# Performance work log

Hardware: AMD Instinct MI355X
Metric: run time of the kernel (lower is better)

## Reference

```python
import jax, jax.numpy as jnp
import numpy as np

B, H, T, D = 2, 16, 2048, 64


def setup_inputs() -> dict:
    key = jax.random.key(0)
    kq, kk, kv, km = jax.random.split(key, 4)
    q = jax.random.normal(kq, (B, H, T, D), dtype=jnp.float32)
    k = jax.random.normal(kk, (B, H, T, D), dtype=jnp.float32)
    v = jax.random.normal(kv, (B, H, T, D), dtype=jnp.float32)
    # boolean mask, True = masked out (broadcast over batch and heads)
    mask = jax.random.randint(km, (1, 1, T, T), 0, 2).astype(jnp.bool_)
    return {"q": q, "k": k, "v": v, "mask": mask}


def reference(q, k, v, mask):
    scale = q.shape[-1] ** (-0.5)
    # [B,H,T,T] score matrix (materialized, as in the original)
    scores = jnp.einsum("bhqd,bhkd->bhqk", q, k) * scale
    scores = jnp.where(mask, jnp.float32(-10000.0), scores)
    attn = jax.nn.softmax(scores, axis=-1)
    attn = jnp.where(mask, jnp.float32(0.0), attn)
    return jnp.einsum("bhqk,bhkd->bhqd", attn, v)
```

## Files before the change

### kernel.cpp

```cpp
#include <hip/hip_runtime.h>
#include <hip/hip_bf16.h>

typedef __bf16 bf16x8 __attribute__((ext_vector_type(8)));
typedef __bf16 bf16x4 __attribute__((ext_vector_type(4)));
typedef float  f32x4  __attribute__((ext_vector_type(4)));
typedef short  s16x4  __attribute__((ext_vector_type(4)));

#define T_SEQ 2048
#define D_HEAD 64
#define BH_N 32
#define SCALE_LOG2 0.18033688011112042f

#define WS_KBF ((size_t)0)
#define WS_VTB ((size_t)8u<<20)
#define WS_MB  ((size_t)16u<<20)

static __device__ inline f32x4 mfma16(bf16x4 a, bf16x4 b, f32x4 c) {
#if __has_builtin(__builtin_amdgcn_mfma_f32_16x16x16_bf16)
    return __builtin_amdgcn_mfma_f32_16x16x16_bf16(a, b, c, 0, 0, 0);
#else
    s16x4 ai = __builtin_bit_cast(s16x4, a);
    s16x4 bi = __builtin_bit_cast(s16x4, b);
    return __builtin_amdgcn_mfma_f32_16x16x16bf16_1k(ai, bi, c, 0, 0, 0);
#endif
}


__global__ __launch_bounds__(256) void prep_kv(const float* __restrict__ k,
                                               const float* __restrict__ v,
                                               __bf16* __restrict__ kb,
                                               __bf16* __restrict__ vt) {
    __shared__ __bf16 t[64][72];
    const int bh = blockIdx.y, tt = blockIdx.x, tid = threadIdx.x;

    {
        const size_t base = ((size_t)bh * T_SEQ + tt * 64 + (tid >> 2)) * D_HEAD + (tid & 3) * 16;
        const float4 a0 = *(const float4*)(k + base);
        const float4 a1 = *(const float4*)(k + base + 4);
        const float4 a2 = *(const float4*)(k + base + 8);
        const float4 a3 = *(const float4*)(k + base + 12);
        bf16x8 w0, w1;
        w0[0]=(__bf16)a0.x; w0[1]=(__bf16)a0.y; w0[2]=(__bf16)a0.z; w0[3]=(__bf16)a0.w;
        w0[4]=(__bf16)a1.x; w0[5]=(__bf16)a1.y; w0[6]=(__bf16)a1.z; w0[7]=(__bf16)a1.w;
        w1[0]=(__bf16)a2.x; w1[1]=(__bf16)a2.y; w1[2]=(__bf16)a2.z; w1[3]=(__bf16)a2.w;
        w1[4]=(__bf16)a3.x; w1[5]=(__bf16)a3.y; w1[6]=(__bf16)a3.z; w1[7]=(__bf16)a3.w;
        *(bf16x8*)(kb + base)     = w0;
        *(bf16x8*)(kb + base + 8) = w1;
    }
    {
        const int tr = tid >> 4, c4 = (tid & 15) * 4;
        const float* src = v + ((size_t)bh * T_SEQ + tt * 64) * D_HEAD;
#pragma unroll
        for (int p = 0; p < 4; ++p) {
            const int row = p * 16 + tr;
            const float4 f = *(const float4*)(src + row * D_HEAD + c4);
            t[c4+0][row] = (__bf16)f.x; t[c4+1][row] = (__bf16)f.y;
            t[c4+2][row] = (__bf16)f.z; t[c4+3][row] = (__bf16)f.w;
        }
        __syncthreads();
        const int d = tid >> 2, seg = tid & 3;
        const bf16x8 a = *(bf16x8*)&t[d][seg * 16];
        const bf16x8 b = *(bf16x8*)&t[d][seg * 16 + 8];
        __bf16* dst = vt + ((size_t)bh * D_HEAD + d) * T_SEQ + tt * 64 + seg * 16;
        *(bf16x8*)dst = a; *(bf16x8*)(dst + 8) = b;
    }
}

__global__ void mpack(const int* __restrict__ m, unsigned long long* __restrict__ mb) {
    const int i = blockIdx.x * 256 + threadIdx.x;
    const unsigned long long b = __ballot(m[i] != 0);
    if ((threadIdx.x & 63) == 0) mb[i >> 6] = b;
}


__global__ __launch_bounds__(128, 2) void attn5(
    const float* __restrict__ q, const __bf16* __restrict__ kb,
    const __bf16* __restrict__ vt, const unsigned long long* __restrict__ mb,
    float* __restrict__ out)
{
    const int qt = blockIdx.x;
    const int bh = blockIdx.y;
    const int tid = threadIdx.x, wave = tid >> 6, lane = tid & 63;
    const int g = lane >> 4, ln = lane & 15;

    __shared__ __align__(16) __bf16 Kl[2][64 * 64];
    __shared__ __align__(16) __bf16 Vl[2][64 * 64];
    __shared__ float ls[2][32];

    const int qw = qt * 64 + wave * 32;

    bf16x8 qf[2][2];
#pragma unroll
    for (int qs = 0; qs < 2; ++qs) {
        const float* qp = q + ((size_t)bh * T_SEQ + qw + qs * 16 + ln) * D_HEAD + g * 8;
#pragma unroll
        for (int kc = 0; kc < 2; ++kc) {
            const float4 f0 = *(const float4*)(qp + kc * 32);
            const float4 f1 = *(const float4*)(qp + kc * 32 + 4);
            qf[qs][kc][0]=(__bf16)(f0.x*SCALE_LOG2); qf[qs][kc][1]=(__bf16)(f0.y*SCALE_LOG2);
            qf[qs][kc][2]=(__bf16)(f0.z*SCALE_LOG2); qf[qs][kc][3]=(__bf16)(f0.w*SCALE_LOG2);
            qf[qs][kc][4]=(__bf16)(f1.x*SCALE_LOG2); qf[qs][kc][5]=(__bf16)(f1.y*SCALE_LOG2);
            qf[qs][kc][6]=(__bf16)(f1.z*SCALE_LOG2); qf[qs][kc][7]=(__bf16)(f1.w*SCALE_LOG2);
        }
    }

    f32x4 o[2][4];
#pragma unroll
    for (int qs = 0; qs < 2; ++qs)
#pragma unroll
        for (int mt = 0; mt < 4; ++mt) o[qs][mt] = (f32x4){0.f, 0.f, 0.f, 0.f};
    float lsum[2] = {0.f, 0.f};

    const int kr = tid >> 1, h = tid & 1;
    const int kwb = kr * 128, ke = kr & 7, ve = kr & 15;
    const __bf16* kbase = kb + (size_t)bh * T_SEQ * D_HEAD;
    const __bf16* vbase = vt + (size_t)bh * D_HEAD * T_SEQ;
    const unsigned long long* mrow0 = mb + (size_t)(qw + ln) * 32;
    const unsigned long long* mrow1 = mb + (size_t)(qw + 16 + ln) * 32;

    char* KlB = (char*)Kl;
    char* VlB = (char*)Vl;

    bf16x8 kn[4], vn[4];

    {
        const __bf16* kp = kbase + (size_t)kr * D_HEAD + h * 32;
        kn[0]=*(const bf16x8*)kp;      kn[1]=*(const bf16x8*)(kp+8);
        kn[2]=*(const bf16x8*)(kp+16); kn[3]=*(const bf16x8*)(kp+24);
        const __bf16* vp = vbase + (size_t)kr * T_SEQ + h * 32;
        vn[0]=*(const bf16x8*)vp;      vn[1]=*(const bf16x8*)(vp+8);
        vn[2]=*(const bf16x8*)(vp+16); vn[3]=*(const bf16x8*)(vp+24);
    }
    unsigned long long mw0 = mrow0[0], mw1 = mrow1[0];
    {
        char* KB = KlB; char* VB = VlB;
#pragma unroll
        for (int i = 0; i < 4; ++i)
            *(bf16x8*)(KB + kwb + (((4*h + i) ^ ke) << 4)) = kn[i];
#pragma unroll
        for (int i = 0; i < 4; ++i) {
            const bf16x4 lo = __builtin_shufflevector(vn[i], vn[i], 0, 1, 2, 3);
            const bf16x4 hi = __builtin_shufflevector(vn[i], vn[i], 4, 5, 6, 7);
            *(bf16x4*)(VB + kwb + (((8*h + 2*i)     ^ ve) << 3)) = lo;
            *(bf16x4*)(VB + kwb + (((8*h + 2*i + 1) ^ ve) << 3)) = hi;
        }
    }
    __syncthreads();

    const int rbK = ln * 128 + ((g ^ (ln & 7)) << 4);

    for (int kt = 0; kt < T_SEQ / 64; ++kt) {
        const int b = kt & 1;
        unsigned long long mn0 = 0, mn1 = 0;
        if (kt < 31) {
            const __bf16* kp = kbase + (size_t)((kt + 1) * 64 + kr) * D_HEAD + h * 32;
            kn[0]=*(const bf16x8*)kp;      kn[1]=*(const bf16x8*)(kp+8);
            kn[2]=*(const bf16x8*)(kp+16); kn[3]=*(const bf16x8*)(kp+24);
            const __bf16* vp = vbase + (size_t)kr * T_SEQ + (kt + 1) * 64 + h * 32;
            vn[0]=*(const bf16x8*)vp;      vn[1]=*(const bf16x8*)(vp+8);
            vn[2]=*(const bf16x8*)(vp+16); vn[3]=*(const bf16x8*)(vp+24);
            mn0 = mrow0[kt + 1]; mn1 = mrow1[kt + 1];
        }

        const char* KB = KlB + b * 8192;
        const char* VB = VlB + b * 8192;

        const unsigned long long s0 = mw0 >> (g * 4), s1 = mw1 >> (g * 4);
        const unsigned int mlo[2] = {(unsigned)s0, (unsigned)s1};
        const unsigned int mhi[2] = {(unsigned)(s0 >> 32), (unsigned)(s1 >> 32)};

        bf16x4 pa[2][4];
#pragma unroll
        for (int nt = 0; nt < 4; ++nt) {
            const bf16x8 a0 = *(const bf16x8*)(KB + nt * 2048 + rbK);
            const bf16x8 a1 = *(const bf16x8*)(KB + nt * 2048 + (rbK ^ 64));
#pragma unroll
            for (int qs = 0; qs < 2; ++qs) {
                f32x4 c = (f32x4){0.f, 0.f, 0.f, 0.f};
                c = __builtin_amdgcn_mfma_f32_16x16x32_bf16(a0, qf[qs][0], c, 0, 0, 0);
                c = __builtin_amdgcn_mfma_f32_16x16x32_bf16(a1, qf[qs][1], c, 0, 0, 0);
                const unsigned int bits = (nt < 2) ? mlo[qs] : mhi[qs];
                float p[4];
#pragma unroll
                for (int r = 0; r < 4; ++r) {
                    const float e = exp2f(c[r]);
                    p[r] = (bits & (1u << ((nt & 1) * 16 + r))) ? 0.f : e;
                }
                lsum[qs] += (p[0] + p[1]) + (p[2] + p[3]);
                pa[qs][nt] = (bf16x4){ (__bf16)p[0], (__bf16)p[1], (__bf16)p[2], (__bf16)p[3] };
            }
        }

#pragma unroll
        for (int mt = 0; mt < 4; ++mt) {
            bf16x4 vf[4];
#pragma unroll
            for (int nt = 0; nt < 4; ++nt)
                vf[nt] = *(const bf16x4*)(VB + (mt * 16 + ln) * 128 + (((nt * 4 + g) ^ (ln & 15)) << 3));
#pragma unroll
            for (int qs = 0; qs < 2; ++qs)
#pragma unroll
                for (int nt = 0; nt < 4; ++nt)
                    o[qs][mt] = mfma16(pa[qs][nt], vf[nt], o[qs][mt]);
        }

        if (kt < 31) {
            char* KB1 = KlB + (b ^ 1) * 8192;
            char* VB1 = VlB + (b ^ 1) * 8192;
#pragma unroll
            for (int i = 0; i < 4; ++i)
                *(bf16x8*)(KB1 + kwb + (((4*h + i) ^ ke) << 4)) = kn[i];
#pragma unroll
            for (int i = 0; i < 4; ++i) {
                const bf16x4 lo = __builtin_shufflevector(vn[i], vn[i], 0, 1, 2, 3);
                const bf16x4 hi = __builtin_shufflevector(vn[i], vn[i], 4, 5, 6, 7);
                *(bf16x4*)(VB1 + kwb + (((8*h + 2*i)     ^ ve) << 3)) = lo;
                *(bf16x4*)(VB1 + kwb + (((8*h + 2*i + 1) ^ ve) << 3)) = hi;
            }
        }
        __syncthreads();
        mw0 = mn0; mw1 = mn1;
    }

#pragma unroll
    for (int qs = 0; qs < 2; ++qs) {
        float l = lsum[qs];
        l += __shfl_xor(l, 16, 64);
        l += __shfl_xor(l, 32, 64);
        const float inv = (l > 0.f) ? (1.f / l) : 0.f;
        if (g == 0) ls[wave][qs * 16 + ln] = inv;
    }
#pragma unroll
    for (int qs = 0; qs < 2; ++qs) {
#pragma unroll
        for (int r = 0; r < 4; ++r) {
            const float iv = ls[wave][qs * 16 + g * 4 + r];
            float* op = out + ((size_t)bh * T_SEQ + qw + qs * 16 + g * 4 + r) * D_HEAD + ln;
#pragma unroll
            for (int mt = 0; mt < 4; ++mt)
                op[mt * 16] = o[qs][mt][r] * iv;
        }
    }
}

extern "C" void kernel_launch(void* const* d_in, const int* in_sizes, int n_in,
                              void* d_out, int out_size, void* d_ws, size_t ws_size,
                              hipStream_t stream) {
    const float* q    = (const float*)d_in[0];
    const float* k    = (const float*)d_in[1];
    const float* v    = (const float*)d_in[2];
    const int*   mask = (const int*)d_in[3];
    float*       out  = (float*)d_out;

    __bf16* kbf = (__bf16*)((char*)d_ws + WS_KBF);
    __bf16* vtb = (__bf16*)((char*)d_ws + WS_VTB);
    unsigned long long* mbw = (unsigned long long*)((char*)d_ws + WS_MB);

    prep_kv<<<dim3(T_SEQ / 64, BH_N), 256, 0, stream>>>(k, v, kbf, vtb);
    mpack<<<(T_SEQ * T_SEQ) / 256, 256, 0, stream>>>(mask, mbw);
    attn5<<<dim3(T_SEQ / 64, BH_N), 128, 0, stream>>>(q, kbf, vtb, mbw, out);
}
```

Before: 185.7 us.

## Split attention block into four waves of 16 queries and sum rows via MFMA

The attention kernel now runs 256 threads (four waves) per 64-query block, each wave owning 16 query rows instead of 32. That halves per-wave accumulator registers and aims for more waves in flight. The row-sum of probabilities is computed with an extra MFMA against a ones vector, replacing the scalar sum, cross-lane shuffles and shared-memory broadcast. In exchange, each K fragment read from LDS now feeds only one query subtile, so LDS traffic per MFMA goes up, and the row-sum MFMAs add matrix work.

```diff
diff --git a/kernel.cpp b/kernel.cpp
--- a/kernel.cpp
+++ b/kernel.cpp
@@ -73,7 +73,7 @@
 }
 
 
-__global__ __launch_bounds__(128, 2) void attn5(
+__global__ __launch_bounds__(256, 4) void attn6(
     const float* __restrict__ q, const __bf16* __restrict__ kb,
     const __bf16* __restrict__ vt, const unsigned long long* __restrict__ mb,
     float* __restrict__ out)
@@ -85,64 +85,57 @@
 
     __shared__ __align__(16) __bf16 Kl[2][64 * 64];
     __shared__ __align__(16) __bf16 Vl[2][64 * 64];
-    __shared__ float ls[2][32];
-
-    const int qw = qt * 64 + wave * 32;
-
-    bf16x8 qf[2][2];
-#pragma unroll
-    for (int qs = 0; qs < 2; ++qs) {
-        const float* qp = q + ((size_t)bh * T_SEQ + qw + qs * 16 + ln) * D_HEAD + g * 8;
+
+    const int qw = qt * 64 + wave * 16;
+
+    bf16x8 qf[2];
+    {
+        const float* qp = q + ((size_t)bh * T_SEQ + qw + ln) * D_HEAD + g * 8;
 #pragma unroll
         for (int kc = 0; kc < 2; ++kc) {
             const float4 f0 = *(const float4*)(qp + kc * 32);
             const float4 f1 = *(const float4*)(qp + kc * 32 + 4);
-            qf[qs][kc][0]=(__bf16)(f0.x*SCALE_LOG2); qf[qs][kc][1]=(__bf16)(f0.y*SCALE_LOG2);
-            qf[qs][kc][2]=(__bf16)(f0.z*SCALE_LOG2); qf[qs][kc][3]=(__bf16)(f0.w*SCALE_LOG2);
-            qf[qs][kc][4]=(__bf16)(f1.x*SCALE_LOG2); qf[qs][kc][5]=(__bf16)(f1.y*SCALE_LOG2);
-            qf[qs][kc][6]=(__bf16)(f1.z*SCALE_LOG2); qf[qs][kc][7]=(__bf16)(f1.w*SCALE_LOG2);
-        }
-    }
-
-    f32x4 o[2][4];
-#pragma unroll
-    for (int qs = 0; qs < 2; ++qs)
-#pragma unroll
-        for (int mt = 0; mt < 4; ++mt) o[qs][mt] = (f32x4){0.f, 0.f, 0.f, 0.f};
-    float lsum[2] = {0.f, 0.f};
-
-    const int kr = tid >> 1, h = tid & 1;
+            qf[kc][0]=(__bf16)(f0.x*SCALE_LOG2); qf[kc][1]=(__bf16)(f0.y*SCALE_LOG2);
+            qf[kc][2]=(__bf16)(f0.z*SCALE_LOG2); qf[kc][3]=(__bf16)(f0.w*SCALE_LOG2);
+            qf[kc][4]=(__bf16)(f1.x*SCALE_LOG2); qf[kc][5]=(__bf16)(f1.y*SCALE_LOG2);
+            qf[kc][6]=(__bf16)(f1.z*SCALE_LOG2); qf[kc][7]=(__bf16)(f1.w*SCALE_LOG2);
+        }
+    }
+
+    f32x4 o[4];
+#pragma unroll
+    for (int mt = 0; mt < 4; ++mt) o[mt] = (f32x4){0.f, 0.f, 0.f, 0.f};
+    f32x4 osum = (f32x4){0.f, 0.f, 0.f, 0.f};
+    const bf16x4 ones = { (__bf16)1.0f, (__bf16)1.0f, (__bf16)1.0f, (__bf16)1.0f };
+
+    const int kr = tid >> 2, qd = tid & 3;
     const int kwb = kr * 128, ke = kr & 7, ve = kr & 15;
     const __bf16* kbase = kb + (size_t)bh * T_SEQ * D_HEAD;
     const __bf16* vbase = vt + (size_t)bh * D_HEAD * T_SEQ;
-    const unsigned long long* mrow0 = mb + (size_t)(qw + ln) * 32;
-    const unsigned long long* mrow1 = mb + (size_t)(qw + 16 + ln) * 32;
+    const unsigned long long* mrow = mb + (size_t)(qw + ln) * 32;
 
     char* KlB = (char*)Kl;
     char* VlB = (char*)Vl;
 
-    bf16x8 kn[4], vn[4];
-
-    {
-        const __bf16* kp = kbase + (size_t)kr * D_HEAD + h * 32;
-        kn[0]=*(const bf16x8*)kp;      kn[1]=*(const bf16x8*)(kp+8);
-        kn[2]=*(const bf16x8*)(kp+16); kn[3]=*(const bf16x8*)(kp+24);
-        const __bf16* vp = vbase + (size_t)kr * T_SEQ + h * 32;
-        vn[0]=*(const bf16x8*)vp;      vn[1]=*(const bf16x8*)(vp+8);
-        vn[2]=*(const bf16x8*)(vp+16); vn[3]=*(const bf16x8*)(vp+24);
-    }
-    unsigned long long mw0 = mrow0[0], mw1 = mrow1[0];
-    {
-        char* KB = KlB; char* VB = VlB;
-#pragma unroll
-        for (int i = 0; i < 4; ++i)
-            *(bf16x8*)(KB + kwb + (((4*h + i) ^ ke) << 4)) = kn[i];
-#pragma unroll
-        for (int i = 0; i < 4; ++i) {
+    bf16x8 kn[2], vn[2];
+
+    {
+        const __bf16* kp = kbase + (size_t)kr * D_HEAD + qd * 16;
+        kn[0] = *(const bf16x8*)kp; kn[1] = *(const bf16x8*)(kp + 8);
+        const __bf16* vp = vbase + (size_t)kr * T_SEQ + qd * 16;
+        vn[0] = *(const bf16x8*)vp; vn[1] = *(const bf16x8*)(vp + 8);
+    }
+    unsigned long long mw = mrow[0];
+    {
+#pragma unroll
+        for (int i = 0; i < 2; ++i)
+            *(bf16x8*)(KlB + kwb + (((2*qd + i) ^ ke) << 4)) = kn[i];
+#pragma unroll
+        for (int i = 0; i < 2; ++i) {
             const bf16x4 lo = __builtin_shufflevector(vn[i], vn[i], 0, 1, 2, 3);
             const bf16x4 hi = __builtin_shufflevector(vn[i], vn[i], 4, 5, 6, 7);
-            *(bf16x4*)(VB + kwb + (((8*h + 2*i)     ^ ve) << 3)) = lo;
-            *(bf16x4*)(VB + kwb + (((8*h + 2*i + 1) ^ ve) << 3)) = hi;
+            *(bf16x4*)(VlB + kwb + (((4*qd + 2*i)     ^ ve) << 3)) = lo;
+            *(bf16x4*)(VlB + kwb + (((4*qd + 2*i + 1) ^ ve) << 3)) = hi;
         }
     }
     __syncthreads();
@@ -151,45 +144,42 @@
 
     for (int kt = 0; kt < T_SEQ / 64; ++kt) {
         const int b = kt & 1;
-        unsigned long long mn0 = 0, mn1 = 0;
+        unsigned long long mn = 0;
         if (kt < 31) {
-            const __bf16* kp = kbase + (size_t)((kt + 1) * 64 + kr) * D_HEAD + h * 32;
-            kn[0]=*(const bf16x8*)kp;      kn[1]=*(const bf16x8*)(kp+8);
-            kn[2]=*(const bf16x8*)(kp+16); kn[3]=*(const bf16x8*)(kp+24);
-            const __bf16* vp = vbase + (size_t)kr * T_SEQ + (kt + 1) * 64 + h * 32;
-            vn[0]=*(const bf16x8*)vp;      vn[1]=*(const bf16x8*)(vp+8);
-            vn[2]=*(const bf16x8*)(vp+16); vn[3]=*(const bf16x8*)(vp+24);
-            mn0 = mrow0[kt + 1]; mn1 = mrow1[kt + 1];
+            const __bf16* kp = kbase + (size_t)((kt + 1) * 64 + kr) * D_HEAD + qd * 16;
+            kn[0] = *(const bf16x8*)kp; kn[1] = *(const bf16x8*)(kp + 8);
+            const __bf16* vp = vbase + (size_t)kr * T_SEQ + (kt + 1) * 64 + qd * 16;
+            vn[0] = *(const bf16x8*)vp; vn[1] = *(const bf16x8*)(vp + 8);
+            mn = mrow[kt + 1];
         }
 
         const char* KB = KlB + b * 8192;
         const char* VB = VlB + b * 8192;
 
-        const unsigned long long s0 = mw0 >> (g * 4), s1 = mw1 >> (g * 4);
-        const unsigned int mlo[2] = {(unsigned)s0, (unsigned)s1};
-        const unsigned int mhi[2] = {(unsigned)(s0 >> 32), (unsigned)(s1 >> 32)};
-
-        bf16x4 pa[2][4];
+        const unsigned long long s = mw >> (g * 4);
+        const unsigned int mlo = (unsigned)s, mhi = (unsigned)(s >> 32);
+
+        bf16x4 pa[4];
 #pragma unroll
         for (int nt = 0; nt < 4; ++nt) {
             const bf16x8 a0 = *(const bf16x8*)(KB + nt * 2048 + rbK);
             const bf16x8 a1 = *(const bf16x8*)(KB + nt * 2048 + (rbK ^ 64));
-#pragma unroll
-            for (int qs = 0; qs < 2; ++qs) {
-                f32x4 c = (f32x4){0.f, 0.f, 0.f, 0.f};
-                c = __builtin_amdgcn_mfma_f32_16x16x32_bf16(a0, qf[qs][0], c, 0, 0, 0);
-                c = __builtin_amdgcn_mfma_f32_16x16x32_bf16(a1, qf[qs][1], c, 0, 0, 0);
-                const unsigned int bits = (nt < 2) ? mlo[qs] : mhi[qs];
-                float p[4];
-#pragma unroll
-                for (int r = 0; r < 4; ++r) {
-                    const float e = exp2f(c[r]);
-                    p[r] = (bits & (1u << ((nt & 1) * 16 + r))) ? 0.f : e;
-                }
-                lsum[qs] += (p[0] + p[1]) + (p[2] + p[3]);
-                pa[qs][nt] = (bf16x4){ (__bf16)p[0], (__bf16)p[1], (__bf16)p[2], (__bf16)p[3] };
+            f32x4 c = (f32x4){0.f, 0.f, 0.f, 0.f};
+            c = __builtin_amdgcn_mfma_f32_16x16x32_bf16(a0, qf[0], c, 0, 0, 0);
+            c = __builtin_amdgcn_mfma_f32_16x16x32_bf16(a1, qf[1], c, 0, 0, 0);
+            const unsigned int bits = (nt < 2) ? mlo : mhi;
+            float p[4];
+#pragma unroll
+            for (int r = 0; r < 4; ++r) {
+                const float e = exp2f(c[r]);
+                p[r] = (bits & (1u << ((nt & 1) * 16 + r))) ? 0.f : e;
             }
-        }
+            pa[nt] = (bf16x4){ (__bf16)p[0], (__bf16)p[1], (__bf16)p[2], (__bf16)p[3] };
+        }
+
+#pragma unroll
+        for (int nt = 0; nt < 4; ++nt)
+            osum = mfma16(pa[nt], ones, osum);
 
 #pragma unroll
         for (int mt = 0; mt < 4; ++mt) {
@@ -198,48 +188,36 @@
             for (int nt = 0; nt < 4; ++nt)
                 vf[nt] = *(const bf16x4*)(VB + (mt * 16 + ln) * 128 + (((nt * 4 + g) ^ (ln & 15)) << 3));
 #pragma unroll
-            for (int qs = 0; qs < 2; ++qs)
-#pragma unroll
-                for (int nt = 0; nt < 4; ++nt)
-                    o[qs][mt] = mfma16(pa[qs][nt], vf[nt], o[qs][mt]);
+            for (int nt = 0; nt < 4; ++nt)
+                o[mt] = mfma16(pa[nt], vf[nt], o[mt]);
         }
 
         if (kt < 31) {
             char* KB1 = KlB + (b ^ 1) * 8192;
             char* VB1 = VlB + (b ^ 1) * 8192;
 #pragma unroll
-            for (int i = 0; i < 4; ++i)
-                *(bf16x8*)(KB1 + kwb + (((4*h + i) ^ ke) << 4)) = kn[i];
-#pragma unroll
-            for (int i = 0; i < 4; ++i) {
+            for (int i = 0; i < 2; ++i)
+                *(bf16x8*)(KB1 + kwb + (((2*qd + i) ^ ke) << 4)) = kn[i];
+#pragma unroll
+            for (int i = 0; i < 2; ++i) {
                 const bf16x4 lo = __builtin_shufflevector(vn[i], vn[i], 0, 1, 2, 3);
                 const bf16x4 hi = __builtin_shufflevector(vn[i], vn[i], 4, 5, 6, 7);
-                *(bf16x4*)(VB1 + kwb + (((8*h + 2*i)     ^ ve) << 3)) = lo;
-                *(bf16x4*)(VB1 + kwb + (((8*h + 2*i + 1) ^ ve) << 3)) = hi;
+                *(bf16x4*)(VB1 + kwb + (((4*qd + 2*i)     ^ ve) << 3)) = lo;
+                *(bf16x4*)(VB1 + kwb + (((4*qd + 2*i + 1) ^ ve) << 3)) = hi;
             }
         }
         __syncthreads();
-        mw0 = mn0; mw1 = mn1;
-    }
-
-#pragma unroll
-    for (int qs = 0; qs < 2; ++qs) {
-        float l = lsum[qs];
-        l += __shfl_xor(l, 16, 64);
-        l += __shfl_xor(l, 32, 64);
+        mw = mn;
+    }
+
+#pragma unroll
+    for (int r = 0; r < 4; ++r) {
+        const float l = osum[r];
         const float inv = (l > 0.f) ? (1.f / l) : 0.f;
-        if (g == 0) ls[wave][qs * 16 + ln] = inv;
-    }
-#pragma unroll
-    for (int qs = 0; qs < 2; ++qs) {
-#pragma unroll
-        for (int r = 0; r < 4; ++r) {
-            const float iv = ls[wave][qs * 16 + g * 4 + r];
-            float* op = out + ((size_t)bh * T_SEQ + qw + qs * 16 + g * 4 + r) * D_HEAD + ln;
-#pragma unroll
-            for (int mt = 0; mt < 4; ++mt)
-                op[mt * 16] = o[qs][mt][r] * iv;
-        }
+        float* op = out + ((size_t)bh * T_SEQ + qw + g * 4 + r) * D_HEAD + ln;
+#pragma unroll
+        for (int mt = 0; mt < 4; ++mt)
+            op[mt * 16] = o[mt][r] * inv;
     }
 }
 
@@ -258,5 +236,5 @@
 
     prep_kv<<<dim3(T_SEQ / 64, BH_N), 256, 0, stream>>>(k, v, kbf, vtb);
     mpack<<<(T_SEQ * T_SEQ) / 256, 256, 0, stream>>>(mask, mbw);
-    attn5<<<dim3(T_SEQ / 64, BH_N), 128, 0, stream>>>(q, kbf, vtb, mbw, out);
-}
+    attn6<<<dim3(T_SEQ / 64, BH_N), 256, 0, stream>>>(q, kbf, vtb, mbw, out);
+}
```

Result: faster. 177.5 us (-4.4%).

## Split key tile across wave pairs with 256-thread blocks and LDS reduction

Applied to the files above, without the earlier changes.

Doubles the block to four waves, with pairs of waves each handling half of every 64-key tile for the same 32 queries, then sums the partial outputs and row sums through shared memory at the end. Row sums are now computed with an MFMA against a ones vector instead of scalar adds. Masking uses a branch-free bitwise AND, and exp2 goes through the hardware intrinsic. The V shared-memory layout is reswizzled for single 16-byte reads. This aims to raise occupancy and cut per-wave VALU work. The cost is an extra epilogue reduction through LDS and more blocks competing for LDS.

```diff
diff --git a/kernel.cpp b/kernel.cpp
--- a/kernel.cpp
+++ b/kernel.cpp
@@ -25,6 +25,14 @@
 #endif
 }
 
+static __device__ inline float fast_exp2(float x) {
+#if __has_builtin(__builtin_amdgcn_exp2f)
+    return __builtin_amdgcn_exp2f(x);
+#else
+    return exp2f(x);
+#endif
+}
+
 
 __global__ __launch_bounds__(256) void prep_kv(const float* __restrict__ k,
                                                const float* __restrict__ v,
@@ -32,7 +40,6 @@
                                                __bf16* __restrict__ vt) {
     __shared__ __bf16 t[64][72];
     const int bh = blockIdx.y, tt = blockIdx.x, tid = threadIdx.x;
-
     {
         const size_t base = ((size_t)bh * T_SEQ + tt * 64 + (tid >> 2)) * D_HEAD + (tid & 3) * 16;
         const float4 a0 = *(const float4*)(k + base);
@@ -73,7 +80,7 @@
 }
 
 
-__global__ __launch_bounds__(128, 2) void attn5(
+__global__ __launch_bounds__(256, 4) void attn8(
     const float* __restrict__ q, const __bf16* __restrict__ kb,
     const __bf16* __restrict__ vt, const unsigned long long* __restrict__ mb,
     float* __restrict__ out)
@@ -82,21 +89,24 @@
     const int bh = blockIdx.y;
     const int tid = threadIdx.x, wave = tid >> 6, lane = tid & 63;
     const int g = lane >> 4, ln = lane & 15;
-
-    __shared__ __align__(16) __bf16 Kl[2][64 * 64];
-    __shared__ __align__(16) __bf16 Vl[2][64 * 64];
-    __shared__ float ls[2][32];
-
-    const int qw = qt * 64 + wave * 32;
+    const int qp = wave & 1, kh = wave >> 1;
+
+    __shared__ __align__(16) char smem[33280];
+    char* KlB = smem;
+    char* VlB = smem + 16384;
+    float* Ep = (float*)smem;
+    float* Os = (float*)(smem + 32768);
+
+    const int qw = qt * 64 + qp * 32;
 
     bf16x8 qf[2][2];
 #pragma unroll
     for (int qs = 0; qs < 2; ++qs) {
-        const float* qp = q + ((size_t)bh * T_SEQ + qw + qs * 16 + ln) * D_HEAD + g * 8;
+        const float* qpt = q + ((size_t)bh * T_SEQ + qw + qs * 16 + ln) * D_HEAD + g * 8;
 #pragma unroll
         for (int kc = 0; kc < 2; ++kc) {
-            const float4 f0 = *(const float4*)(qp + kc * 32);
-            const float4 f1 = *(const float4*)(qp + kc * 32 + 4);
+            const float4 f0 = *(const float4*)(qpt + kc * 32);
+            const float4 f1 = *(const float4*)(qpt + kc * 32 + 4);
             qf[qs][kc][0]=(__bf16)(f0.x*SCALE_LOG2); qf[qs][kc][1]=(__bf16)(f0.y*SCALE_LOG2);
             qf[qs][kc][2]=(__bf16)(f0.z*SCALE_LOG2); qf[qs][kc][3]=(__bf16)(f0.w*SCALE_LOG2);
             qf[qs][kc][4]=(__bf16)(f1.x*SCALE_LOG2); qf[qs][kc][5]=(__bf16)(f1.y*SCALE_LOG2);
@@ -109,114 +119,111 @@
     for (int qs = 0; qs < 2; ++qs)
 #pragma unroll
         for (int mt = 0; mt < 4; ++mt) o[qs][mt] = (f32x4){0.f, 0.f, 0.f, 0.f};
-    float lsum[2] = {0.f, 0.f};
-
-    const int kr = tid >> 1, h = tid & 1;
-    const int kwb = kr * 128, ke = kr & 7, ve = kr & 15;
+    f32x4 osum[2] = { (f32x4){0.f,0.f,0.f,0.f}, (f32x4){0.f,0.f,0.f,0.f} };
+    const bf16x4 ones = { (__bf16)1.0f, (__bf16)1.0f, (__bf16)1.0f, (__bf16)1.0f };
+
+    const int kr = tid >> 2, qd = tid & 3;
+    const int kwb = kr * 128, ke = kr & 7;
     const __bf16* kbase = kb + (size_t)bh * T_SEQ * D_HEAD;
     const __bf16* vbase = vt + (size_t)bh * D_HEAD * T_SEQ;
     const unsigned long long* mrow0 = mb + (size_t)(qw + ln) * 32;
     const unsigned long long* mrow1 = mb + (size_t)(qw + 16 + ln) * 32;
 
-    char* KlB = (char*)Kl;
-    char* VlB = (char*)Vl;
-
-    bf16x8 kn[4], vn[4];
-
-    {
-        const __bf16* kp = kbase + (size_t)kr * D_HEAD + h * 32;
-        kn[0]=*(const bf16x8*)kp;      kn[1]=*(const bf16x8*)(kp+8);
-        kn[2]=*(const bf16x8*)(kp+16); kn[3]=*(const bf16x8*)(kp+24);
-        const __bf16* vp = vbase + (size_t)kr * T_SEQ + h * 32;
-        vn[0]=*(const bf16x8*)vp;      vn[1]=*(const bf16x8*)(vp+8);
-        vn[2]=*(const bf16x8*)(vp+16); vn[3]=*(const bf16x8*)(vp+24);
+    bf16x8 kn[2], vn[2];
+
+    {
+        const __bf16* kp = kbase + (size_t)kr * D_HEAD + qd * 16;
+        kn[0] = *(const bf16x8*)kp; kn[1] = *(const bf16x8*)(kp + 8);
+        const __bf16* vp = vbase + (size_t)kr * T_SEQ + qd * 16;
+        vn[0] = *(const bf16x8*)vp; vn[1] = *(const bf16x8*)(vp + 8);
     }
     unsigned long long mw0 = mrow0[0], mw1 = mrow1[0];
     {
-        char* KB = KlB; char* VB = VlB;
-#pragma unroll
-        for (int i = 0; i < 4; ++i)
-            *(bf16x8*)(KB + kwb + (((4*h + i) ^ ke) << 4)) = kn[i];
-#pragma unroll
-        for (int i = 0; i < 4; ++i) {
-            const bf16x4 lo = __builtin_shufflevector(vn[i], vn[i], 0, 1, 2, 3);
-            const bf16x4 hi = __builtin_shufflevector(vn[i], vn[i], 4, 5, 6, 7);
-            *(bf16x4*)(VB + kwb + (((8*h + 2*i)     ^ ve) << 3)) = lo;
-            *(bf16x4*)(VB + kwb + (((8*h + 2*i + 1) ^ ve) << 3)) = hi;
-        }
+        *(bf16x8*)(KlB + kwb + (((2*qd + 0) ^ ke) << 4)) = kn[0];
+        *(bf16x8*)(KlB + kwb + (((2*qd + 1) ^ ke) << 4)) = kn[1];
+#pragma unroll
+        for (int c = 0; c < 2; ++c)
+#pragma unroll
+            for (int gg = 0; gg < 2; ++gg) {
+                const int g2 = c * 2 + gg;
+                const int gran = (g2 << 1) | (qd >> 1);
+                const bf16x4 part = gg ? __builtin_shufflevector(vn[c], vn[c], 4,5,6,7)
+                                       : __builtin_shufflevector(vn[c], vn[c], 0,1,2,3);
+                *(bf16x4*)(VlB + kwb + ((gran ^ ke) << 4) + ((qd & 1) << 3)) = part;
+            }
     }
     __syncthreads();
-
-    const int rbK = ln * 128 + ((g ^ (ln & 7)) << 4);
 
     for (int kt = 0; kt < T_SEQ / 64; ++kt) {
         const int b = kt & 1;
         unsigned long long mn0 = 0, mn1 = 0;
         if (kt < 31) {
-            const __bf16* kp = kbase + (size_t)((kt + 1) * 64 + kr) * D_HEAD + h * 32;
-            kn[0]=*(const bf16x8*)kp;      kn[1]=*(const bf16x8*)(kp+8);
-            kn[2]=*(const bf16x8*)(kp+16); kn[3]=*(const bf16x8*)(kp+24);
-            const __bf16* vp = vbase + (size_t)kr * T_SEQ + (kt + 1) * 64 + h * 32;
-            vn[0]=*(const bf16x8*)vp;      vn[1]=*(const bf16x8*)(vp+8);
-            vn[2]=*(const bf16x8*)(vp+16); vn[3]=*(const bf16x8*)(vp+24);
+            const __bf16* kp = kbase + (size_t)((kt + 1) * 64 + kr) * D_HEAD + qd * 16;
+            kn[0] = *(const bf16x8*)kp; kn[1] = *(const bf16x8*)(kp + 8);
+            const __bf16* vp = vbase + (size_t)kr * T_SEQ + (kt + 1) * 64 + qd * 16;
+            vn[0] = *(const bf16x8*)vp; vn[1] = *(const bf16x8*)(vp + 8);
             mn0 = mrow0[kt + 1]; mn1 = mrow1[kt + 1];
         }
 
         const char* KB = KlB + b * 8192;
         const char* VB = VlB + b * 8192;
 
-        const unsigned long long s0 = mw0 >> (g * 4), s1 = mw1 >> (g * 4);
-        const unsigned int mlo[2] = {(unsigned)s0, (unsigned)s1};
-        const unsigned int mhi[2] = {(unsigned)(s0 >> 32), (unsigned)(s1 >> 32)};
-
-        bf16x4 pa[2][4];
-#pragma unroll
-        for (int nt = 0; nt < 4; ++nt) {
-            const bf16x8 a0 = *(const bf16x8*)(KB + nt * 2048 + rbK);
-            const bf16x8 a1 = *(const bf16x8*)(KB + nt * 2048 + (rbK ^ 64));
+        const unsigned nbs0 = (~(unsigned)(mw0 >> (kh << 5))) >> (g * 4);
+        const unsigned nbs1 = (~(unsigned)(mw1 >> (kh << 5))) >> (g * 4);
+
+        bf16x4 pa[2][2];
+#pragma unroll
+        for (int ntl = 0; ntl < 2; ++ntl) {
+            const int row = (2 * kh + ntl) * 16 + ln;
+            const int rb = row * 128 + ((g ^ (ln & 7)) << 4);
+            const bf16x8 a0 = *(const bf16x8*)(KB + rb);
+            const bf16x8 a1 = *(const bf16x8*)(KB + (rb ^ 64));
 #pragma unroll
             for (int qs = 0; qs < 2; ++qs) {
                 f32x4 c = (f32x4){0.f, 0.f, 0.f, 0.f};
                 c = __builtin_amdgcn_mfma_f32_16x16x32_bf16(a0, qf[qs][0], c, 0, 0, 0);
                 c = __builtin_amdgcn_mfma_f32_16x16x32_bf16(a1, qf[qs][1], c, 0, 0, 0);
-                const unsigned int bits = (nt < 2) ? mlo[qs] : mhi[qs];
+                const unsigned nbs = qs ? nbs1 : nbs0;
                 float p[4];
 #pragma unroll
                 for (int r = 0; r < 4; ++r) {
-                    const float e = exp2f(c[r]);
-                    p[r] = (bits & (1u << ((nt & 1) * 16 + r))) ? 0.f : e;
+                    const float e = fast_exp2(c[r]);
+                    const int keep = (int)(nbs << (31 - (ntl * 16 + r))) >> 31;
+                    p[r] = __builtin_bit_cast(float, __builtin_bit_cast(unsigned, e) & (unsigned)keep);
                 }
-                lsum[qs] += (p[0] + p[1]) + (p[2] + p[3]);
-                pa[qs][nt] = (bf16x4){ (__bf16)p[0], (__bf16)p[1], (__bf16)p[2], (__bf16)p[3] };
+                pa[qs][ntl] = (bf16x4){ (__bf16)p[0], (__bf16)p[1], (__bf16)p[2], (__bf16)p[3] };
+                osum[qs] = mfma16(pa[qs][ntl], ones, osum[qs]);
             }
         }
 
 #pragma unroll
         for (int mt = 0; mt < 4; ++mt) {
-            bf16x4 vf[4];
-#pragma unroll
-            for (int nt = 0; nt < 4; ++nt)
-                vf[nt] = *(const bf16x4*)(VB + (mt * 16 + ln) * 128 + (((nt * 4 + g) ^ (ln & 15)) << 3));
-#pragma unroll
-            for (int qs = 0; qs < 2; ++qs)
-#pragma unroll
-                for (int nt = 0; nt < 4; ++nt)
-                    o[qs][mt] = mfma16(pa[qs][nt], vf[nt], o[qs][mt]);
+            const int vrow = mt * 16 + ln;
+            const bf16x8 vv = *(const bf16x8*)(VB + vrow * 128 + ((((g << 1) | kh) ^ (ln & 7)) << 4));
+            const bf16x4 vf0 = __builtin_shufflevector(vv, vv, 0, 1, 2, 3);
+            const bf16x4 vf1 = __builtin_shufflevector(vv, vv, 4, 5, 6, 7);
+#pragma unroll
+            for (int qs = 0; qs < 2; ++qs) {
+                o[qs][mt] = mfma16(pa[qs][0], vf0, o[qs][mt]);
+                o[qs][mt] = mfma16(pa[qs][1], vf1, o[qs][mt]);
+            }
         }
 
         if (kt < 31) {
             char* KB1 = KlB + (b ^ 1) * 8192;
             char* VB1 = VlB + (b ^ 1) * 8192;
-#pragma unroll
-            for (int i = 0; i < 4; ++i)
-                *(bf16x8*)(KB1 + kwb + (((4*h + i) ^ ke) << 4)) = kn[i];
-#pragma unroll
-            for (int i = 0; i < 4; ++i) {
-                const bf16x4 lo = __builtin_shufflevector(vn[i], vn[i], 0, 1, 2, 3);
-                const bf16x4 hi = __builtin_shufflevector(vn[i], vn[i], 4, 5, 6, 7);
-                *(bf16x4*)(VB1 + kwb + (((8*h + 2*i)     ^ ve) << 3)) = lo;
-                *(bf16x4*)(VB1 + kwb + (((8*h + 2*i + 1) ^ ve) << 3)) = hi;
-            }
+            *(bf16x8*)(KB1 + kwb + (((2*qd + 0) ^ ke) << 4)) = kn[0];
+            *(bf16x8*)(KB1 + kwb + (((2*qd + 1) ^ ke) << 4)) = kn[1];
+#pragma unroll
+            for (int c = 0; c < 2; ++c)
+#pragma unroll
+                for (int gg = 0; gg < 2; ++gg) {
+                    const int g2 = c * 2 + gg;
+                    const int gran = (g2 << 1) | (qd >> 1);
+                    const bf16x4 part = gg ? __builtin_shufflevector(vn[c], vn[c], 4,5,6,7)
+                                           : __builtin_shufflevector(vn[c], vn[c], 0,1,2,3);
+                    *(bf16x4*)(VB1 + kwb + ((gran ^ ke) << 4) + ((qd & 1) << 3)) = part;
+                }
         }
         __syncthreads();
         mw0 = mn0; mw1 = mn1;
@@ -224,22 +231,29 @@
 
 #pragma unroll
     for (int qs = 0; qs < 2; ++qs) {
-        float l = lsum[qs];
-        l += __shfl_xor(l, 16, 64);
-        l += __shfl_xor(l, 32, 64);
+#pragma unroll
+        for (int mt = 0; mt < 4; ++mt)
+#pragma unroll
+            for (int r = 0; r < 4; ++r)
+                Ep[(size_t)kh * 4096 + (qp * 32 + qs * 16 + g * 4 + r) * 64 + mt * 16 + ln] = o[qs][mt][r];
+        if (ln == 0) {
+#pragma unroll
+            for (int r = 0; r < 4; ++r)
+                Os[kh * 64 + qp * 32 + qs * 16 + g * 4 + r] = osum[qs][r];
+        }
+    }
+    __syncthreads();
+#pragma unroll
+    for (int p = 0; p < 4; ++p) {
+        const int idx = p * 256 + tid;
+        const int row = idx >> 4, c4 = (idx & 15) * 4;
+        const float l = Os[row] + Os[64 + row];
         const float inv = (l > 0.f) ? (1.f / l) : 0.f;
-        if (g == 0) ls[wave][qs * 16 + ln] = inv;
-    }
-#pragma unroll
-    for (int qs = 0; qs < 2; ++qs) {
-#pragma unroll
-        for (int r = 0; r < 4; ++r) {
-            const float iv = ls[wave][qs * 16 + g * 4 + r];
-            float* op = out + ((size_t)bh * T_SEQ + qw + qs * 16 + g * 4 + r) * D_HEAD + ln;
-#pragma unroll
-            for (int mt = 0; mt < 4; ++mt)
-                op[mt * 16] = o[qs][mt][r] * iv;
-        }
+        const float4 a  = *(const float4*)(Ep + row * 64 + c4);
+        const float4 b4 = *(const float4*)(Ep + 4096 + row * 64 + c4);
+        const float4 st = { (a.x + b4.x) * inv, (a.y + b4.y) * inv,
+                            (a.z + b4.z) * inv, (a.w + b4.w) * inv };
+        *(float4*)(out + ((size_t)bh * T_SEQ + qt * 64 + row) * D_HEAD + c4) = st;
     }
 }
 
@@ -258,5 +272,5 @@
 
     prep_kv<<<dim3(T_SEQ / 64, BH_N), 256, 0, stream>>>(k, v, kbf, vtb);
     mpack<<<(T_SEQ * T_SEQ) / 256, 256, 0, stream>>>(mask, mbw);
-    attn5<<<dim3(T_SEQ / 64, BH_N), 128, 0, stream>>>(q, kbf, vtb, mbw, out);
-}
+    attn8<<<dim3(T_SEQ / 64, BH_N), 256, 0, stream>>>(q, kbf, vtb, mbw, out);
+}
```

Result: faster. 166.8 us (-10.2%).
